# Performance work log

Hardware: AMD Instinct MI355X
Metric: run time of the kernel (lower is better)

## Reference

```python
import jax, jax.numpy as jnp
import numpy as np

B, L, C, H = 2, 4096, 1024, 16
D = C // H
KERNEL_FROM_KN = lambda kn: int(np.sqrt(kn)) + 1


def setup_inputs() -> dict:
    key = jax.random.key(0)
    ks = jax.random.split(key, 4)
    s = 0.02
    kk = KERNEL_FROM_KN(144)  # 13
    return {
        "x": jax.random.normal(ks[0], (B, L, C), jnp.float32),
        "w_qkv": jax.random.normal(ks[1], (C, 3 * C), jnp.float32) * s,
        "b_qkv": jnp.zeros((3 * C,), jnp.float32),
        "rpb": jax.random.normal(ks[2], (H, 2 * kk - 1), jnp.float32) * s,
        "w_proj": jax.random.normal(ks[3], (C, C), jnp.float32) * s,
        "b_proj": jnp.zeros((C,), jnp.float32),
        "k_neighbors": 144,
    }


def reference(x, w_qkv, b_qkv, rpb, w_proj, b_proj, k_neighbors):
    kk = KERNEL_FROM_KN(k_neighbors)  # kernel size (13)
    scale = D ** -0.5
    qkv = (x @ w_qkv + b_qkv).reshape(B, L, 3, H, D).transpose(2, 0, 3, 1, 4)  # (3,B,H,L,D)
    q, k, v = qkv[0] * scale, qkv[1], qkv[2]
    pos = jnp.arange(L)
    # NATTEN window: centered, clamped so the full kernel fits inside [0, L)
    start = jnp.clip(pos - kk // 2, 0, L - kk)               # (L,)
    idx = start[:, None] + jnp.arange(kk)[None, :]           # (L,kk) key positions
    k_win = k[:, :, idx, :]                                  # (B,H,L,kk,D)
    v_win = v[:, :, idx, :]                                  # (B,H,L,kk,D)
    attn = jnp.einsum('bhld,bhlkd->bhlk', q, k_win)          # (B,H,L,kk)
    # relative-position bias index = key_pos - query_pos + (kk - 1) in [0, 2kk-2]
    bias_idx = idx - pos[:, None] + (kk - 1)                 # (L,kk)
    attn = attn + rpb[:, bias_idx][None]                     # broadcast over batch
    attn = jax.nn.softmax(attn, axis=-1)
    out = jnp.einsum('bhlk,bhlkd->bhld', attn, v_win)        # (B,H,L,D)
    out = out.transpose(0, 2, 1, 3).reshape(B, L, C)
    return out @ w_proj + b_proj
```

## Files before the change

kernel.cpp:

```cpp
#include <hip/hip_runtime.h>
#include <hip/hip_bf16.h>
#include <stdint.h>

typedef __bf16 bf16x8 __attribute__((ext_vector_type(8)));
typedef float floatx4 __attribute__((ext_vector_type(4)));

#define B_ 2
#define L_ 4096
#define C_ 1024
#define H_ 16
#define D_ 64
constexpr size_t TEN = (size_t)B_ * H_ * L_ * D_;

__device__ __forceinline__ float bf2f(unsigned short u) {
  union { unsigned int i; float f; } x; x.i = ((unsigned int)u) << 16; return x.f;
}
__device__ __forceinline__ unsigned short f2bf(float f) {
  union { float f; unsigned int i; } x; x.f = f;
  unsigned int i = x.i;
  return (unsigned short)((i + 0x7FFFu + ((i >> 16) & 1u)) >> 16);
}

__device__ __forceinline__ void async_copy16(const unsigned short* g, unsigned short* l) {
  __builtin_amdgcn_global_load_lds(
      (const __attribute__((address_space(1))) unsigned int*)g,
      (__attribute__((address_space(3))) unsigned int*)l,
      16, 0, 0);
}

__global__ __launch_bounds__(256) void cvt_f32_bf16_kernel(
    const float* __restrict__ in, unsigned short* __restrict__ out, int n) {
  int i = (blockIdx.x * 256 + threadIdx.x) * 8;
  if (i >= n) return;
  float4 a = *(const float4*)&in[i];
  float4 b = *(const float4*)&in[i + 4];
  union { uint4 u; unsigned short s[8]; } st;
  st.s[0] = f2bf(a.x); st.s[1] = f2bf(a.y); st.s[2] = f2bf(a.z); st.s[3] = f2bf(a.w);
  st.s[4] = f2bf(b.x); st.s[5] = f2bf(b.y); st.s[6] = f2bf(b.z); st.s[7] = f2bf(b.w);
  *(uint4*)&out[i] = st.u;
}

__global__ __launch_bounds__(256) void transpose_f32_bf16(
    const float* __restrict__ in, unsigned short* __restrict__ out,
    int R, int Ccols) {
  __shared__ float tile[64][65];
  const int bx = blockIdx.x * 64;
  const int by = blockIdx.y * 64;
  const int t = threadIdx.x;
  for (int i = t; i < 1024; i += 256) {
    int r = i >> 4, c4 = (i & 15) << 2;
    float4 v = *(const float4*)&in[(size_t)(by + r) * Ccols + bx + c4];
    tile[r][c4] = v.x; tile[r][c4 + 1] = v.y; tile[r][c4 + 2] = v.z; tile[r][c4 + 3] = v.w;
  }
  __syncthreads();
  for (int i = t; i < 512; i += 256) {
    int r = i >> 3, c8 = (i & 7) << 3;
    union { uint4 u; unsigned short s[8]; } st;
    #pragma unroll
    for (int j = 0; j < 8; ++j) st.s[j] = f2bf(tile[c8 + j][r]);
    *(uint4*)&out[(size_t)(bx + r) * R + by + c8] = st.u;
  }
}

template <int MODE>
__global__ __launch_bounds__(256) void gemm_bt_kernel(
    const unsigned short* __restrict__ A, const unsigned short* __restrict__ Bt,
    const float* __restrict__ bias, unsigned short* __restrict__ out_bf,
    float* __restrict__ out_f, int M, int N, int K, float qscale) {
  constexpr int BK = 64;
  __shared__ unsigned short a_sh[128 * BK];
  __shared__ unsigned short b_sh[128 * BK];

  const int t = threadIdx.x;
  const int m0 = blockIdx.y * 128;
  const int n0 = blockIdx.x * 128;
  const int wave = t >> 6, lane = t & 63;
  const int wr = wave >> 1, wc = wave & 1;
  const int lm = lane & 15, quad = lane >> 4;

  const int soff = t * 8;
  const int srow = soff >> 6;
  const int scol = soff & 63;

  floatx4 acc[4][4];
  #pragma unroll
  for (int i = 0; i < 4; ++i)
    #pragma unroll
    for (int j = 0; j < 4; ++j) acc[i][j] = (floatx4)0.0f;

  for (int kt = 0; kt < K; kt += BK) {
    #pragma unroll
    for (int p = 0; p < 4; ++p) {
      int r = srow + p * 32;
      int off = r * BK + scol;
      async_copy16(&A[(size_t)(m0 + r) * K + kt + scol], &a_sh[off]);
      async_copy16(&Bt[(size_t)(n0 + r) * K + kt + scol], &b_sh[off]);
    }
    __syncthreads();
    #pragma unroll
    for (int ks = 0; ks < BK; ks += 32) {
      bf16x8 af[4], bfr[4];
      #pragma unroll
      for (int i = 0; i < 4; ++i)
        af[i] = *(const bf16x8*)&a_sh[(wr * 64 + i * 16 + lm) * BK + ks + quad * 8];
      #pragma unroll
      for (int j = 0; j < 4; ++j)
        bfr[j] = *(const bf16x8*)&b_sh[(wc * 64 + j * 16 + lm) * BK + ks + quad * 8];
      #pragma unroll
      for (int i = 0; i < 4; ++i)
        #pragma unroll
        for (int j = 0; j < 4; ++j)
          acc[i][j] = __builtin_amdgcn_mfma_f32_16x16x32_bf16(af[i], bfr[j], acc[i][j], 0, 0, 0);
    }
    __syncthreads();
  }

  #pragma unroll
  for (int j = 0; j < 4; ++j) {
    int col = n0 + wc * 64 + j * 16 + lm;
    float bv = bias[col];
    if (MODE == 0) {
      int which = col >> 10;
      int rem = col & 1023;
      int h = rem >> 6, d = rem & 63;
      float mul = (which == 0) ? qscale : 1.0f;
      #pragma unroll
      for (int i = 0; i < 4; ++i)
        #pragma unroll
        for (int r = 0; r < 4; ++r) {
          int row = m0 + wr * 64 + i * 16 + quad * 4 + r;
          int b = row >> 12, l = row & (L_ - 1);
          float v = (acc[i][j][r] + bv) * mul;
          out_bf[(size_t)which * TEN + (((size_t)(b * H_ + h) * L_ + l) * D_ + d)] = f2bf(v);
        }
    } else {
      #pragma unroll
      for (int i = 0; i < 4; ++i)
        #pragma unroll
        for (int r = 0; r < 4; ++r) {
          int row = m0 + wr * 64 + i * 16 + quad * 4 + r;
          out_f[(size_t)row * N + col] = acc[i][j][r] + bv;
        }
    }
  }
}

constexpr int KKMAX = 63;
constexpr int TL = 128;
constexpr int LDK = 72;

__global__ __launch_bounds__(256) void natt_kernel(
    const unsigned short* __restrict__ qkv,
    const float* __restrict__ rpb,
    const int* __restrict__ knp,
    unsigned short* __restrict__ attn_out) {
  __shared__ unsigned short k_sh[(TL + KKMAX) * LDK];
  __shared__ unsigned short v_sh[(TL + KKMAX) * LDK];
  __shared__ float rpb_sh[2 * KKMAX + 1];

  const int bh = blockIdx.x;
  const int h = bh & (H_ - 1);
  const int b = bh >> 4;
  const int l0 = blockIdx.y * TL;
  const int t = threadIdx.x;

  int kn = knp[0];
  if (kn > 65536 || kn < 0) {
    union { int i; float f; } u; u.i = kn; kn = (int)u.f;
  }
  int rr = 1;
  while ((rr + 1) * (rr + 1) <= kn) ++rr;
  int kk = rr + 1;
  if (kk > KKMAX) kk = KKMAX;

  int base = l0 - kk / 2;
  if (base < 0) base = 0;
  if (base > L_ - kk) base = L_ - kk;
  int nrows = TL + kk;
  if (nrows > L_ - base) nrows = L_ - base;

  const unsigned short* kg = qkv + TEN + (size_t)bh * L_ * D_;
  const unsigned short* vg = qkv + 2 * TEN + (size_t)bh * L_ * D_;

  for (int i = t; i < nrows * 8; i += 256) {
    int row = i >> 3, c8 = (i & 7) << 3;
    uint4 kv = *(const uint4*)&kg[(size_t)(base + row) * D_ + c8];
    *(uint4*)&k_sh[row * LDK + c8] = kv;
    uint4 vv = *(const uint4*)&vg[(size_t)(base + row) * D_ + c8];
    *(uint4*)&v_sh[row * LDK + c8] = vv;
  }
  int nb = 2 * kk - 1;
  for (int i = t; i < nb; i += 256) rpb_sh[i] = rpb[h * nb + i];
  __syncthreads();

  const int qi = t >> 1, half = t & 1;
  const int l = l0 + qi;

  const unsigned short* qg = qkv + (size_t)bh * L_ * D_ + (size_t)l * D_ + half * 32;
  float qv[32];
  #pragma unroll
  for (int c = 0; c < 4; ++c) {
    union { uint4 u; unsigned short s[8]; } ld;
    ld.u = *(const uint4*)&qg[c * 8];
    #pragma unroll
    for (int j = 0; j < 8; ++j) qv[c * 8 + j] = bf2f(ld.s[j]);
  }

  int start = l - kk / 2;
  if (start < 0) start = 0;
  if (start > L_ - kk) start = L_ - kk;
  const int srow = start - base;
  const int boff = start - l + kk - 1;

  float m = -1e30f, lsum = 0.0f;
  float accv[32];
  #pragma unroll
  for (int d = 0; d < 32; ++d) accv[d] = 0.0f;

  for (int j = 0; j < kk; ++j) {
    const unsigned short* kr = &k_sh[(srow + j) * LDK + half * 32];
    float partial = 0.0f;
    #pragma unroll
    for (int c = 0; c < 4; ++c) {
      union { uint4 u; unsigned short s[8]; } ld;
      ld.u = *(const uint4*)&kr[c * 8];
      #pragma unroll
      for (int jj = 0; jj < 8; ++jj) partial += qv[c * 8 + jj] * bf2f(ld.s[jj]);
    }
    float s = partial + __shfl_xor(partial, 1) + rpb_sh[boff + j];
    float p;
    if (s > m) {
      float corr = __expf(m - s);
      lsum *= corr;
      #pragma unroll
      for (int d = 0; d < 32; ++d) accv[d] *= corr;
      m = s;
      p = 1.0f;
    } else {
      p = __expf(s - m);
    }
    lsum += p;
    const unsigned short* vr = &v_sh[(srow + j) * LDK + half * 32];
    #pragma unroll
    for (int c = 0; c < 4; ++c) {
      union { uint4 u; unsigned short s[8]; } ld;
      ld.u = *(const uint4*)&vr[c * 8];
      #pragma unroll
      for (int jj = 0; jj < 8; ++jj) accv[c * 8 + jj] += p * bf2f(ld.s[jj]);
    }
  }
  float inv = 1.0f / lsum;
  unsigned short* og = attn_out + ((size_t)(b * L_ + l) * C_ + h * D_ + half * 32);
  #pragma unroll
  for (int c = 0; c < 4; ++c) {
    union { uint4 u; unsigned short s[8]; } st;
    #pragma unroll
    for (int jj = 0; jj < 8; ++jj) st.s[jj] = f2bf(accv[c * 8 + jj] * inv);
    *(uint4*)&og[c * 8] = st.u;
  }
}

extern "C" void kernel_launch(void* const* d_in, const int* in_sizes, int n_in,
                              void* d_out, int out_size, void* d_ws, size_t ws_size,
                              hipStream_t stream) {
  const float* x      = (const float*)d_in[0];
  const float* w_qkv  = (const float*)d_in[1];
  const float* b_qkv  = (const float*)d_in[2];
  const float* rpb    = (const float*)d_in[3];
  const float* w_proj = (const float*)d_in[4];
  const float* b_proj = (const float*)d_in[5];
  const int* kn       = (const int*)d_in[6];
  float* out          = (float*)d_out;

  unsigned short* ws      = (unsigned short*)d_ws;
  unsigned short* wT_qkv  = ws;
  unsigned short* wT_proj = wT_qkv + (size_t)3072 * 1024;
  unsigned short* x_bf    = wT_proj + (size_t)1024 * 1024;
  unsigned short* qkv_ws  = x_bf + (size_t)8192 * 1024;
  unsigned short* attn_ws = qkv_ws + 3 * TEN;

  cvt_f32_bf16_kernel<<<(8192 * 1024) / (256 * 8), 256, 0, stream>>>(x, x_bf, 8192 * 1024);
  transpose_f32_bf16<<<dim3(3072 / 64, 1024 / 64), 256, 0, stream>>>(w_qkv, wT_qkv, 1024, 3072);
  transpose_f32_bf16<<<dim3(1024 / 64, 1024 / 64), 256, 0, stream>>>(w_proj, wT_proj, 1024, 1024);
  gemm_bt_kernel<0><<<dim3(3072 / 128, 8192 / 128), 256, 0, stream>>>(
      x_bf, wT_qkv, b_qkv, qkv_ws, nullptr, 8192, 3072, 1024, 0.125f);
  natt_kernel<<<dim3(B_ * H_, L_ / TL), 256, 0, stream>>>(qkv_ws, rpb, kn, attn_ws);
  gemm_bt_kernel<1><<<dim3(1024 / 128, 8192 / 128), 256, 0, stream>>>(
      attn_ws, wT_proj, b_proj, nullptr, out, 8192, 1024, 1024, 1.0f);
}
```

Before: 238.9 us.

## Pipeline GEMM K-loop with 4-stage async LDS buffers, XOR swizzle, and tile remap

The GEMM main loop now uses four LDS buffers for A and B and prefetches three K-tiles ahead with async global-to-LDS copies. Each step waits on vmcnt and a single barrier instead of two syncthreads per tile, so loads overlap with the MFMA work. LDS columns are XOR-swizzled by row to cut bank conflicts. Workgroups are remapped in groups of eight, likely for cache locality. The loop is hardcoded to 16 K-tiles (K=1024), which assumes every call has K equal to C, and LDS use grows fourfold, which may lower occupancy.

```diff
diff --git a/kernel.cpp b/kernel.cpp
--- a/kernel.cpp
+++ b/kernel.cpp
@@ -68,52 +68,85 @@
     const float* __restrict__ bias, unsigned short* __restrict__ out_bf,
     float* __restrict__ out_f, int M, int N, int K, float qscale) {
   constexpr int BK = 64;
-  __shared__ unsigned short a_sh[128 * BK];
-  __shared__ unsigned short b_sh[128 * BK];
+  constexpr int TE = 128 * BK;
+  __shared__ unsigned short a_sh0[TE], a_sh1[TE], a_sh2[TE], a_sh3[TE];
+  __shared__ unsigned short b_sh0[TE], b_sh1[TE], b_sh2[TE], b_sh3[TE];
 
   const int t = threadIdx.x;
-  const int m0 = blockIdx.y * 128;
-  const int n0 = blockIdx.x * 128;
+  const int nwgx = gridDim.x;
+  const int nwg = nwgx * gridDim.y;
+  const int flat = blockIdx.y * nwgx + blockIdx.x;
+  const int cpx = nwg >> 3;
+  const int swz = (flat & 7) * cpx + (flat >> 3);
+  const int m0 = (swz / nwgx) * 128;
+  const int n0 = (swz % nwgx) * 128;
+
   const int wave = t >> 6, lane = t & 63;
   const int wr = wave >> 1, wc = wave & 1;
   const int lm = lane & 15, quad = lane >> 4;
 
-  const int soff = t * 8;
-  const int srow = soff >> 6;
-  const int scol = soff & 63;
-
   floatx4 acc[4][4];
   #pragma unroll
   for (int i = 0; i < 4; ++i)
     #pragma unroll
     for (int j = 0; j < 4; ++j) acc[i][j] = (floatx4)0.0f;
 
-  for (int kt = 0; kt < K; kt += BK) {
-    #pragma unroll
-    for (int p = 0; p < 4; ++p) {
-      int r = srow + p * 32;
-      int off = r * BK + scol;
-      async_copy16(&A[(size_t)(m0 + r) * K + kt + scol], &a_sh[off]);
-      async_copy16(&Bt[(size_t)(n0 + r) * K + kt + scol], &b_sh[off]);
-    }
-    __syncthreads();
-    #pragma unroll
-    for (int ks = 0; ks < BK; ks += 32) {
-      bf16x8 af[4], bfr[4];
-      #pragma unroll
-      for (int i = 0; i < 4; ++i)
-        af[i] = *(const bf16x8*)&a_sh[(wr * 64 + i * 16 + lm) * BK + ks + quad * 8];
-      #pragma unroll
-      for (int j = 0; j < 4; ++j)
-        bfr[j] = *(const bf16x8*)&b_sh[(wc * 64 + j * 16 + lm) * BK + ks + quad * 8];
-      #pragma unroll
-      for (int i = 0; i < 4; ++i)
-        #pragma unroll
-        for (int j = 0; j < 4; ++j)
-          acc[i][j] = __builtin_amdgcn_mfma_f32_16x16x32_bf16(af[i], bfr[j], acc[i][j], 0, 0, 0);
-    }
-    __syncthreads();
-  }
+#define STAGE_TILE(TT, SA, SB) do { \
+    int kt_ = (TT) * BK; \
+    _Pragma("unroll") \
+    for (int p = 0; p < 4; ++p) { \
+      int off = (p * 256 + t) * 8; \
+      int r_ = off >> 6; \
+      int c_ = (off & 63) ^ ((r_ & 7) << 3); \
+      async_copy16(&A[(size_t)(m0 + r_) * K + kt_ + c_], &SA[off]); \
+      async_copy16(&Bt[(size_t)(n0 + r_) * K + kt_ + c_], &SB[off]); \
+    } \
+  } while (0)
+
+#define KSTEP(TT, ASH, BSH, SA, SB, DO_ST, VMC) do { \
+    asm volatile("s_waitcnt vmcnt(" #VMC ")" ::: "memory"); \
+    __builtin_amdgcn_s_barrier(); \
+    asm volatile("" ::: "memory"); \
+    if (DO_ST) STAGE_TILE((TT) + 3, SA, SB); \
+    _Pragma("unroll") \
+    for (int ks = 0; ks < BK; ks += 32) { \
+      bf16x8 af[4], bfr[4]; \
+      _Pragma("unroll") \
+      for (int i = 0; i < 4; ++i) { \
+        int ra = wr * 64 + i * 16 + lm; \
+        af[i] = *(const bf16x8*)&ASH[ra * 64 + ((ks + quad * 8) ^ ((ra & 7) << 3))]; \
+      } \
+      _Pragma("unroll") \
+      for (int j = 0; j < 4; ++j) { \
+        int rb = wc * 64 + j * 16 + lm; \
+        bfr[j] = *(const bf16x8*)&BSH[rb * 64 + ((ks + quad * 8) ^ ((rb & 7) << 3))]; \
+      } \
+      _Pragma("unroll") \
+      for (int i = 0; i < 4; ++i) \
+        _Pragma("unroll") \
+        for (int j = 0; j < 4; ++j) \
+          acc[i][j] = __builtin_amdgcn_mfma_f32_16x16x32_bf16(af[i], bfr[j], acc[i][j], 0, 0, 0); \
+    } \
+  } while (0)
+
+  STAGE_TILE(0, a_sh0, b_sh0);
+  STAGE_TILE(1, a_sh1, b_sh1);
+  STAGE_TILE(2, a_sh2, b_sh2);
+
+  for (int g = 0; g < 3; ++g) {
+    int tb = g * 4;
+    KSTEP(tb + 0, a_sh0, b_sh0, a_sh3, b_sh3, true, 16);
+    KSTEP(tb + 1, a_sh1, b_sh1, a_sh0, b_sh0, true, 16);
+    KSTEP(tb + 2, a_sh2, b_sh2, a_sh1, b_sh1, true, 16);
+    KSTEP(tb + 3, a_sh3, b_sh3, a_sh2, b_sh2, true, 16);
+  }
+  KSTEP(12, a_sh0, b_sh0, a_sh3, b_sh3, true, 16);
+  KSTEP(13, a_sh1, b_sh1, a_sh0, b_sh0, false, 16);
+  KSTEP(14, a_sh2, b_sh2, a_sh0, b_sh0, false, 8);
+  KSTEP(15, a_sh3, b_sh3, a_sh0, b_sh0, false, 0);
+
+#undef KSTEP
+#undef STAGE_TILE
 
   #pragma unroll
   for (int j = 0; j < 4; ++j) {
```

New measurement: 232.5 us. 2.7% less time.
